# Performance work log

Measured on AMD Instinct MI355X. Metric: run time of the kernel, lower is better.

The kernel has to match this reference:

```python
import jax, jax.numpy as jnp
import numpy as np

DIM = 1024
INTER = 512
E = 32            # n_routed_experts
TOPK = 4          # n_activated_experts
GROUPS = 8        # n_expert_groups
TOPK_GROUPS = 4
SHARED_INTER = 2 * INTER  # n_shared_experts * moe_inter_dim
ROUTE_SCALE = 1.0
B, S = 8, 4096


def setup_inputs() -> dict:
    key = jax.random.key(0)
    ks = jax.random.split(key, 16)
    def xav(k, shape):
        fan_in, fan_out = shape[-2], shape[-1]
        lim = np.sqrt(6.0 / (fan_in + fan_out))
        return jax.random.uniform(k, shape, jnp.float32, -lim, lim)
    return {
        "x": jax.random.normal(ks[0], (B, S, DIM), jnp.float32),
        "gw": xav(ks[1], (DIM, E)),
        "gb": jnp.zeros((E,), jnp.float32),
        "w1": xav(ks[2], (E, DIM, INTER)),
        "b1": jnp.zeros((E, INTER), jnp.float32),
        "w3": xav(ks[3], (E, DIM, INTER)),
        "b3": jnp.zeros((E, INTER), jnp.float32),
        "w2": xav(ks[4], (E, INTER, DIM)),
        "b2": jnp.zeros((E, DIM), jnp.float32),
        "sw1": xav(ks[5], (DIM, SHARED_INTER)),
        "sb1": jnp.zeros((SHARED_INTER,), jnp.float32),
        "sw3": xav(ks[6], (DIM, SHARED_INTER)),
        "sb3": jnp.zeros((SHARED_INTER,), jnp.float32),
        "sw2": xav(ks[7], (SHARED_INTER, DIM)),
        "sb2": jnp.zeros((DIM,), jnp.float32),
    }


def _gate(xf, gw, gb):
    # scores: softmax over routed experts in fp32 (score_func='softmax')
    T = xf.shape[0]
    scores = jax.nn.softmax((xf @ gw + gb).astype(jnp.float32), axis=-1)  # [T, E]
    original_scores = scores
    # group-masked routing (n_expert_groups > 1)
    scores_g = scores.reshape(T, GROUPS, E // GROUPS)                     # [T, G, E/G]
    group_scores = jnp.sum(jax.lax.top_k(scores_g, 2)[0], axis=-1)        # [T, G]
    gidx = jax.lax.top_k(group_scores, TOPK_GROUPS)[1]                    # [T, topk_groups]
    keep = jnp.zeros((T, GROUPS), bool).at[jnp.arange(T)[:, None], gidx].set(True)
    masked = jnp.where(keep[:, :, None], scores_g, -jnp.inf).reshape(T, E)
    indices = jax.lax.top_k(masked, TOPK)[1]                              # [T, topk]
    weights = jnp.take_along_axis(original_scores, indices, axis=1) * ROUTE_SCALE
    return weights.astype(xf.dtype), indices


def reference(x, gw, gb, w1, b1, w3, b3, w2, b2, sw1, sb1, sw3, sb3, sw2, sb2):
    shape = x.shape
    xf = x.reshape(-1, DIM)                                               # [T, dim]
    T = xf.shape[0]
    weights, indices = _gate(xf, gw, gb)
    # dense combine weights [T, E]: w_e(t) = routing weight if expert e chosen for t else 0
    cw = jnp.zeros((T, E), xf.dtype).at[jnp.arange(T)[:, None], indices].add(weights)
    # scan over experts: y += w_e * SwiGLU_e(x). Zero weight -> zero contribution,
    # identical math to the masked dispatch/scatter-add in the torch code.
    def body(y, p):
        w1e, b1e, w3e, b3e, w2e, b2e, we = p
        h = jax.nn.silu(xf @ w1e + b1e) * (xf @ w3e + b3e)                # [T, inter]
        return y + we[:, None] * (h @ w2e + b2e), None
    y0 = jnp.zeros_like(xf)
    y, _ = jax.lax.scan(body, y0, (w1, b1, w3, b3, w2, b2, cw.T))
    # shared experts MLP (SwiGLU)
    z = (jax.nn.silu(xf @ sw1 + sb1) * (xf @ sw3 + sb3)) @ sw2 + sb2
    return (y + z).reshape(shape)
```

## Files before the change

### kernel.cpp

```cpp
#include <hip/hip_runtime.h>
#include <stdint.h>

#define DIM_    1024
#define INTER_  512

typedef short bf16x4 __attribute__((ext_vector_type(4)));
typedef short bf16x8 __attribute__((ext_vector_type(8)));
typedef float f32x4  __attribute__((ext_vector_type(4)));

__device__ __forceinline__ unsigned short f2bf(float f) {
  union { float f; unsigned u; } v; v.f = f;
  return (unsigned short)((v.u + 0x7FFFu + ((v.u >> 16) & 1u)) >> 16);
}
__device__ __forceinline__ unsigned f2bf2(float a, float b) {
  union { float f; unsigned u; } va, vb; va.f = a; vb.f = b;
  unsigned ra = (va.u + 0x7FFFu + ((va.u >> 16) & 1u)) >> 16;
  unsigned rb = (vb.u + 0x7FFFu + ((vb.u >> 16) & 1u)) >> 16;
  return ra | (rb << 16);
}
__device__ __forceinline__ float bfhi(unsigned u) {
  union { unsigned u; float f; } v; v.u = u & 0xffff0000u; return v.f;
}
__device__ __forceinline__ float bflo(unsigned u) {
  union { unsigned u; float f; } v; v.u = u << 16; return v.f;
}

__device__ __forceinline__ void gl16(const void* g, void* l) {
  __builtin_amdgcn_global_load_lds(
      (const __attribute__((address_space(1))) unsigned int*)g,
      (__attribute__((address_space(3))) unsigned int*)l, 16, 0, 0);
}

#define BARX() do { asm volatile("" ::: "memory"); \
                    __builtin_amdgcn_s_barrier();  \
                    asm volatile("" ::: "memory"); } while (0)

__global__ __launch_bounds__(256) void gate_kernel(
    const float* __restrict__ x, const float* __restrict__ gw,
    const float* __restrict__ gb, int* __restrict__ idx, float* __restrict__ wts,
    unsigned short* __restrict__ xb) {
  __shared__ double s_sc[4][32];
  __shared__ double s_gs[4][8];
  const int wid = threadIdx.x >> 6, lane = threadIdx.x & 63;
  const int t = blockIdx.x * 4 + wid;
  {
    const float* xrow = x + (size_t)t * DIM_ + lane * 16;
    unsigned short* xbrow = xb + (size_t)t * DIM_ + lane * 16;
    float4 f0 = *(const float4*)(xrow);
    float4 f1 = *(const float4*)(xrow + 4);
    float4 f2v = *(const float4*)(xrow + 8);
    float4 f3v = *(const float4*)(xrow + 12);
    uint4 o0, o1;
    o0.x = f2bf2(f0.x, f0.y);  o0.y = f2bf2(f0.z, f0.w);
    o0.z = f2bf2(f1.x, f1.y);  o0.w = f2bf2(f1.z, f1.w);
    o1.x = f2bf2(f2v.x, f2v.y); o1.y = f2bf2(f2v.z, f2v.w);
    o1.z = f2bf2(f3v.x, f3v.y); o1.w = f2bf2(f3v.z, f3v.w);
    *(uint4*)(xbrow) = o0;
    *(uint4*)(xbrow + 8) = o1;
  }
  const int e = lane & 31, half = lane >> 5;
  const float* xr  = x  + (size_t)t * DIM_ + half * 512;
  const float* gwp = gw + (size_t)half * 512 * 32 + e;
  double a0 = 0, a1 = 0, a2 = 0, a3 = 0;
  for (int k = 0; k < 512; k += 4) {
    float4 xv = *(const float4*)(xr + k);
    a0 += (double)xv.x * (double)gwp[(k + 0) * 32];
    a1 += (double)xv.y * (double)gwp[(k + 1) * 32];
    a2 += (double)xv.z * (double)gwp[(k + 2) * 32];
    a3 += (double)xv.w * (double)gwp[(k + 3) * 32];
  }
  double lg = (a0 + a1) + (a2 + a3);
  lg += __shfl_xor(lg, 32);
  lg += (double)gb[e];
  double m = lg;
  #pragma unroll
  for (int d = 1; d < 32; d <<= 1) m = fmax(m, __shfl_xor(m, d));
  double ex = exp(lg - m);
  double ssum = ex;
  #pragma unroll
  for (int d = 1; d < 32; d <<= 1) ssum += __shfl_xor(ssum, d);
  double sc = ex / ssum;
  double p  = __shfl_xor(sc, 1);
  double m1 = fmax(sc, p), n1 = fmin(sc, p);
  double m2 = __shfl_xor(m1, 2), n2 = __shfl_xor(n1, 2);
  double gs = (m1 >= m2) ? (m1 + fmax(n1, m2)) : (m2 + fmax(n2, m1));
  if (lane < 32) {
    s_sc[wid][e] = sc;
    if ((e & 3) == 0) s_gs[wid][e >> 2] = gs;
  }
  __syncthreads();
  if (lane == 0) {
    unsigned kmask = 0;
    for (int it = 0; it < 4; ++it) {
      int bg = 0; double bv = -1.0;
      for (int g = 0; g < 8; ++g)
        if (!((kmask >> g) & 1u) && s_gs[wid][g] > bv) { bv = s_gs[wid][g]; bg = g; }
      kmask |= 1u << bg;
    }
    unsigned umask = 0;
    for (int slot = 0; slot < 4; ++slot) {
      int be = 0; double bv = -1.0;
      for (int ee = 0; ee < 32; ++ee)
        if (((kmask >> (ee >> 2)) & 1u) && !((umask >> ee) & 1u) && s_sc[wid][ee] > bv) {
          bv = s_sc[wid][ee]; be = ee;
        }
      umask |= 1u << be;
      idx[t * 4 + slot] = be;
      wts[t * 4 + slot] = (float)bv;
    }
  }
}

__global__ __launch_bounds__(256) void count_kernel(const int* __restrict__ idx,
                                                    int* __restrict__ meta) {
  __shared__ int h[32];
  int tid = threadIdx.x;
  if (tid < 32) h[tid] = 0;
  __syncthreads();
  atomicAdd(&h[idx[blockIdx.x * 256 + tid]], 1);
  __syncthreads();
  if (tid < 32 && h[tid]) atomicAdd(&meta[tid], h[tid]);
}

__global__ void scan_kernel(int* __restrict__ meta) {
  int lane = threadIdx.x & 63;
  if (lane < 32) {
    int c = meta[lane];
    int pre = c;
    #pragma unroll
    for (int d = 1; d < 32; d <<= 1) { int t = __shfl_up(pre, d); if (lane >= d) pre += t; }
    int excl = pre - c;
    meta[64 + lane] = excl;
    meta[32 + lane] = excl;
    int nt = (c + 255) >> 8;
    int ntp = nt;
    #pragma unroll
    for (int d = 1; d < 32; d <<= 1) { int t = __shfl_up(ntp, d); if (lane >= d) ntp += t; }
    int ntExcl = ntp - nt;
    for (int k = 0; k < nt; ++k) { meta[128 + ntExcl + k] = lane; meta[1184 + ntExcl + k] = k << 8; }
    if (lane == 31) { meta[96] = excl + c; meta[97] = ntExcl + nt; }
  }
}

__global__ __launch_bounds__(256) void scatter_kernel(
    const int* __restrict__ idx, int* __restrict__ meta,
    int* __restrict__ tok, int* __restrict__ inv) {
  int i = blockIdx.x * 256 + threadIdx.x;
  int lane = threadIdx.x & 63;
  int e = idx[i];
  unsigned long long m = ~0ull;
  #pragma unroll
  for (int b = 0; b < 5; ++b) {
    unsigned long long vote = __ballot((e >> b) & 1);
    m &= ((e >> b) & 1) ? vote : ~vote;
  }
  int leader = __ffsll((long long)m) - 1;
  int rank = __popcll(m & ((1ull << lane) - 1));
  int base = 0;
  if (lane == leader) base = atomicAdd(&meta[32 + e], (int)__popcll(m));
  base = __shfl(base, leader);
  int p = base + rank;
  tok[p] = i >> 2;
  inv[i] = p;
}

__global__ __launch_bounds__(256) void repack_kernel(
    const float* __restrict__ src, unsigned short* __restrict__ dst,
    int K, int N, int tilesPerMat) {
  const int w = blockIdx.x * 4 + (threadIdx.x >> 6);
  const int j = threadIdx.x & 63;
  const int e = w / tilesPerMat, rem = w % tilesPerMat;
  const int kSteps = K >> 5;
  const int nt = rem / kSteps, kq = rem % kSteps;
  const float* s = src + (size_t)e * K * N + (size_t)(kq * 32) * N + nt * 64 + j;
  float v[32];
  #pragma unroll
  for (int kk = 0; kk < 32; ++kk) v[kk] = s[(size_t)kk * N];
  char* d = (char*)dst + (size_t)w * 4096 + j * 16;
  #pragma unroll
  for (int q = 0; q < 4; ++q) {
    int o = q * 8;
    uint4 tv;
    tv.x = f2bf2(v[o + 0], v[o + 1]);
    tv.y = f2bf2(v[o + 2], v[o + 3]);
    tv.z = f2bf2(v[o + 4], v[o + 5]);
    tv.w = f2bf2(v[o + 6], v[o + 7]);
    *(uint4*)(d + q * 1024) = tv;
  }
}

__global__ __launch_bounds__(256) void repack13_kernel(
    const float* __restrict__ src1, const float* __restrict__ src3,
    unsigned short* __restrict__ dst, int K, int N, int jtTiles) {
  const int w = blockIdx.x * 4 + (threadIdx.x >> 6);
  const int j = threadIdx.x & 63;
  const int kSteps = K >> 5;
  const int tpm = jtTiles * kSteps;
  const int e = w / tpm, rem = w % tpm;
  const int jt = rem / kSteps, kq = rem % kSteps;
  const int jg = jt * 64 + j;
  const int c = ((jg >> 5) << 4) + (jg & 15);
  const float* s = (((jg >> 4) & 1) ? src3 : src1)
                 + (size_t)e * K * N + (size_t)(kq * 32) * N + c;
  float v[32];
  #pragma unroll
  for (int kk = 0; kk < 32; ++kk) v[kk] = s[(size_t)kk * N];
  char* d = (char*)dst + (size_t)w * 4096 + j * 16;
  #pragma unroll
  for (int q = 0; q < 4; ++q) {
    int o = q * 8;
    uint4 tv;
    tv.x = f2bf2(v[o + 0], v[o + 1]);
    tv.y = f2bf2(v[o + 2], v[o + 3]);
    tv.z = f2bf2(v[o + 4], v[o + 5]);
    tv.w = f2bf2(v[o + 6], v[o + 7]);
    *(uint4*)(d + q * 1024) = tv;
  }
}


#define G4_PRE()                                                              \
  const int tid = threadIdx.x, lane = tid & 63, wave = tid >> 6;              \
  const int wm = wave >> 1, wn = wave & 1;                                    \
  const int f = lane & 15, g = lane >> 4;                                     \
  const int rsg = wave * 16 + (lane >> 2);                                    \
  const int qs = (((lane & 3) ^ ((rsg & 3) ^ ((rsg >> 2) & 3))) << 4);        \
  const int wv1k = wave * 1024;                                               \
  const int bso = (wave & 3) * 1024 + lane * 16;                              \
  int aoff[4], boff[4];                                                       \
  _Pragma("unroll")                                                           \
  for (int ii = 0; ii < 4; ++ii) {                                            \
    int u16 = ii * 16 + f;                                                    \
    aoff[ii] = (wm >> 1) * 8192 + (wm & 1) * 4096 + u16 * 64 +                \
               ((g ^ ((u16 & 3) ^ ((u16 >> 2) & 3))) << 4);                   \
    boff[ii] = 16384 + wn * 4096 + g * 1024 + u16 * 16;                       \
  }                                                                           \
  f32x4 acc[4][4];                                                            \
  const f32x4 zz = {0.f, 0.f, 0.f, 0.f};                                      \
  _Pragma("unroll")                                                           \
  for (int mi = 0; mi < 4; ++mi)                                              \
    _Pragma("unroll")                                                         \
    for (int ni = 0; ni < 4; ++ni) acc[mi][ni] = zz;

#define G4_STAGE(td, u_)                                                      \
  gl16(pA0 + (u_) * 64, (td) + wv1k);                                         \
  gl16(pA1 + (u_) * 64, (td) + 8192 + wv1k);                                  \
  gl16(pB + (size_t)(u_) * 4096, (td) + 16384 + wv1k);

#define G4_BODY(NU)                                                           \
  {                                                                           \
    G4_STAGE(lds, 0);                                                         \
    G4_STAGE(lds + 24576, ((NU) > 1 ? 1 : 0));                                \
    asm volatile("s_waitcnt vmcnt(3)" ::: "memory");                          \
    BARX();                                                                   \
  }                                                                           \
  int bc = 0, bt = 49152;                                                     \
  for (int u = 0; u < (NU); ++u) {                                            \
    int u_ = u + 2; if (u_ > (NU) - 1) u_ = (NU) - 1;                         \
    char* td = lds + bt;                                                      \
    G4_STAGE(td, u_);                                                         \
    const char* cb = lds + bc;                                                \
    bf16x8 af[4], bv[4];                                                      \
    _Pragma("unroll")                                                         \
    for (int mi = 0; mi < 4; ++mi) af[mi] = *(const bf16x8*)(cb + aoff[mi]);  \
    _Pragma("unroll")                                                         \
    for (int ni = 0; ni < 4; ++ni) bv[ni] = *(const bf16x8*)(cb + boff[ni]);  \
    __builtin_amdgcn_s_setprio(1);                                            \
    _Pragma("unroll")                                                         \
    for (int ni = 0; ni < 4; ++ni)                                            \
      _Pragma("unroll")                                                       \
      for (int mi = 0; mi < 4; ++mi)                                          \
        acc[mi][ni] = __builtin_amdgcn_mfma_f32_16x16x32_bf16(                \
            af[mi], bv[ni], acc[mi][ni], 0, 0, 0);                            \
    __builtin_amdgcn_s_setprio(0);                                            \
    asm volatile("s_waitcnt vmcnt(3)" ::: "memory");                          \
    BARX();                                                                   \
    bc = (bc == 49152) ? 0 : bc + 24576;                                      \
    bt = (bt == 49152) ? 0 : bt + 24576;                                      \
  }

#define XCD_SWZ(GXv)                                                          \
  const int nb_ = gridDim.x;                                                  \
  const int b_ = blockIdx.x;                                                  \
  const int w_ = (b_ & 7) * (nb_ >> 3) + (b_ >> 3);                           \
  const int bx = w_ % (GXv);                                                  \
  const int by = w_ / (GXv);

__global__ __launch_bounds__(512, 4) void s1_kernel(
    const unsigned short* __restrict__ xb, const unsigned short* __restrict__ w13,
    const float* __restrict__ sb1, const float* __restrict__ sb3,
    unsigned short* __restrict__ Hs) {
  __shared__ char lds[73728];
  XCD_SWZ(16);
  const int m0 = by * 256;
  G4_PRE();
  const char* pA0 = (const char*)xb + (size_t)(m0 + rsg) * 2048 + qs;
  const char* pA1 = pA0 + (size_t)128 * 2048;
  const char* pB = (const char*)w13 + ((size_t)(bx * 2 + (wave >> 2)) * 32) * 4096 + bso;
  G4_BODY(32);
  const int colb = bx * 64;
  #pragma unroll
  for (int p2 = 0; p2 < 2; ++p2) {
    int c = colb + wn * 32 + p2 * 16 + f;
    float bb1 = sb1[c], bb3 = sb3[c];
    #pragma unroll
    for (int mi = 0; mi < 4; ++mi) {
      int row = m0 + wm * 64 + mi * 16 + g * 4;
      #pragma unroll
      for (int r = 0; r < 4; ++r) {
        float v1 = acc[mi][2 * p2][r] + bb1;
        float v3 = acc[mi][2 * p2 + 1][r] + bb3;
        float h = (v1 / (1.f + __expf(-v1))) * v3;
        Hs[(size_t)(row + r) * 1024 + c] = f2bf(h);
      }
    }
  }
}

__global__ __launch_bounds__(512, 4) void s2_kernel(
    const unsigned short* __restrict__ Hs, const unsigned short* __restrict__ b2i,
    const float* __restrict__ sb2, float* __restrict__ out) {
  __shared__ char lds[73728];
  XCD_SWZ(8);
  const int m0 = by * 256;
  G4_PRE();
  const char* pA0 = (const char*)Hs + (size_t)(m0 + rsg) * 2048 + qs;
  const char* pA1 = pA0 + (size_t)128 * 2048;
  const char* pB = (const char*)b2i + ((size_t)(bx * 2 + (wave >> 2)) * 32) * 4096 + bso;
  G4_BODY(32);
  #pragma unroll
  for (int ni = 0; ni < 4; ++ni) {
    int c = bx * 128 + wn * 64 + ni * 16 + f;
    float bb = sb2[c];
    #pragma unroll
    for (int mi = 0; mi < 4; ++mi) {
      int row = m0 + wm * 64 + mi * 16 + g * 4;
      #pragma unroll
      for (int r = 0; r < 4; ++r)
        out[(size_t)(row + r) * 1024 + c] = acc[mi][ni][r] + bb;
    }
  }
}

__global__ __launch_bounds__(512, 4) void g1_kernel(
    const unsigned short* __restrict__ xb, const unsigned short* __restrict__ w13,
    const float* __restrict__ b1, const float* __restrict__ b3,
    const int* __restrict__ tok, const int* __restrict__ meta,
    unsigned short* __restrict__ H) {
  __shared__ char lds[73728];
  XCD_SWZ(8);
  if (by >= meta[97]) return;
  const int e = meta[128 + by], m0 = meta[1184 + by];
  const int off_e = meta[64 + e], nrem = meta[e] - m0;
  G4_PRE();
  const int ix0 = off_e + m0 + ((rsg < nrem) ? rsg : 0);
  const int ix1 = off_e + m0 + ((rsg + 128 < nrem) ? rsg + 128 : 0);
  const char* pA0 = (const char*)xb + (size_t)tok[ix0] * 2048 + qs;
  const char* pA1 = (const char*)xb + (size_t)tok[ix1] * 2048 + qs;
  const char* pB = (const char*)w13 + ((size_t)(e * 16 + bx * 2 + (wave >> 2)) * 32) * 4096 + bso;
  G4_BODY(32);
  const int colb = bx * 64;
  #pragma unroll
  for (int p2 = 0; p2 < 2; ++p2) {
    int c = colb + wn * 32 + p2 * 16 + f;
    float bb1 = b1[e * 512 + c], bb3 = b3[e * 512 + c];
    #pragma unroll
    for (int mi = 0; mi < 4; ++mi) {
      int row = wm * 64 + mi * 16 + g * 4;
      #pragma unroll
      for (int r = 0; r < 4; ++r) {
        if (row + r < nrem) {
          float v1 = acc[mi][2 * p2][r] + bb1;
          float v3 = acc[mi][2 * p2 + 1][r] + bb3;
          float h = (v1 / (1.f + __expf(-v1))) * v3;
          H[(size_t)(off_e + m0 + row + r) * 512 + c] = f2bf(h);
        }
      }
    }
  }
}

__global__ __launch_bounds__(512, 4) void g2_kernel(
    const unsigned short* __restrict__ H, const unsigned short* __restrict__ w2i,
    const float* __restrict__ b2, const int* __restrict__ meta,
    unsigned short* __restrict__ Y, int cbase) {
  __shared__ char lds[73728];
  XCD_SWZ(4);
  if (by >= meta[97]) return;
  const int e = meta[128 + by], m0 = meta[1184 + by];
  const int off_e = meta[64 + e], nrem = meta[e] - m0;
  G4_PRE();
  const int ix0 = off_e + m0 + ((rsg < nrem) ? rsg : 0);
  const int ix1 = off_e + m0 + ((rsg + 128 < nrem) ? rsg + 128 : 0);
  const char* pA0 = (const char*)H + (size_t)ix0 * 1024 + qs;
  const char* pA1 = (const char*)H + (size_t)ix1 * 1024 + qs;
  const int nt0 = (cbase >> 6) + bx * 2;
  const char* pB = (const char*)w2i + ((size_t)(e * 16 + nt0 + (wave >> 2)) * 16) * 4096 + bso;
  G4_BODY(16);
  #pragma unroll
  for (int ni = 0; ni < 4; ++ni) {
    int ycol = bx * 128 + wn * 64 + ni * 16 + f;
    float bb = b2[e * 1024 + cbase + ycol];
    #pragma unroll
    for (int mi = 0; mi < 4; ++mi) {
      int row = wm * 64 + mi * 16 + g * 4;
      #pragma unroll
      for (int r = 0; r < 4; ++r) {
        if (row + r < nrem)
          Y[(size_t)(off_e + m0 + row + r) * 512 + ycol] = f2bf(acc[mi][ni][r] + bb);
      }
    }
  }
}

__global__ __launch_bounds__(256) void combine_kernel(
    const unsigned short* __restrict__ Y, const int* __restrict__ inv,
    const float* __restrict__ wts, float* __restrict__ out, int cbase) {
  int t = blockIdx.x * 2 + (threadIdx.x >> 7);
  int c = (threadIdx.x & 127) * 4;
  int4 iv = *(const int4*)(inv + t * 4);
  float4 wv = *(const float4*)(wts + t * 4);
  float* op = out + (size_t)t * 1024 + cbase + c;
  float4 o = *(float4*)op;
  uint2 u;
  u = *(const uint2*)(Y + (size_t)iv.x * 512 + c);
  o.x += wv.x * bflo(u.x); o.y += wv.x * bfhi(u.x);
  o.z += wv.x * bflo(u.y); o.w += wv.x * bfhi(u.y);
  u = *(const uint2*)(Y + (size_t)iv.y * 512 + c);
  o.x += wv.y * bflo(u.x); o.y += wv.y * bfhi(u.x);
  o.z += wv.y * bflo(u.y); o.w += wv.y * bfhi(u.y);
  u = *(const uint2*)(Y + (size_t)iv.z * 512 + c);
  o.x += wv.z * bflo(u.x); o.y += wv.z * bfhi(u.x);
  o.z += wv.z * bflo(u.y); o.w += wv.z * bfhi(u.y);
  u = *(const uint2*)(Y + (size_t)iv.w * 512 + c);
  o.x += wv.w * bflo(u.x); o.y += wv.w * bfhi(u.x);
  o.z += wv.w * bflo(u.y); o.w += wv.w * bfhi(u.y);
  *(float4*)op = o;
}

extern "C" void kernel_launch(void* const* d_in, const int* in_sizes, int n_in,
                              void* d_out, int out_size, void* d_ws, size_t ws_size,
                              hipStream_t stream) {
  const float* x   = (const float*)d_in[0];
  const float* gw  = (const float*)d_in[1];
  const float* gb  = (const float*)d_in[2];
  const float* w1  = (const float*)d_in[3];
  const float* b1  = (const float*)d_in[4];
  const float* w3  = (const float*)d_in[5];
  const float* b3  = (const float*)d_in[6];
  const float* w2  = (const float*)d_in[7];
  const float* b2  = (const float*)d_in[8];
  const float* sw1 = (const float*)d_in[9];
  const float* sb1 = (const float*)d_in[10];
  const float* sw3 = (const float*)d_in[11];
  const float* sb3 = (const float*)d_in[12];
  const float* sw2 = (const float*)d_in[13];
  const float* sb2 = (const float*)d_in[14];
  float* out = (float*)d_out;
  char* ws = (char*)d_ws;

  const size_t OFF_XB   = 134217728;
  const size_t OFF_W13I = 201326592;
  const size_t OFF_W2I  = 268435456;
  const size_t OFF_S13I = 301989888;
  const size_t OFF_SW2I = 306184192;
  const size_t OFF_IDX  = 308281344;
  const size_t OFF_WTS  = 308805632;
  const size_t OFF_TOK  = 309329920;
  const size_t OFF_INV  = 309854208;
  const size_t OFF_META = 310378496;
  if (ws_size < OFF_META + 8960) return;

  unsigned short* H    = (unsigned short*)ws;
  unsigned short* xb   = (unsigned short*)(ws + OFF_XB);
  unsigned short* Yb   = (unsigned short*)(ws + OFF_XB);
  unsigned short* w13i = (unsigned short*)(ws + OFF_W13I);
  unsigned short* w2i  = (unsigned short*)(ws + OFF_W2I);
  unsigned short* s13i = (unsigned short*)(ws + OFF_S13I);
  unsigned short* sw2i = (unsigned short*)(ws + OFF_SW2I);
  int*   idx  = (int*)(ws + OFF_IDX);
  float* wts  = (float*)(ws + OFF_WTS);
  int*   tokl = (int*)(ws + OFF_TOK);
  int*   inv  = (int*)(ws + OFF_INV);
  int*   meta = (int*)(ws + OFF_META);

  hipMemsetAsync(meta, 0, 128, stream);
  gate_kernel<<<dim3(8192), dim3(256), 0, stream>>>(x, gw, gb, idx, wts, xb);
  count_kernel<<<dim3(512), dim3(256), 0, stream>>>(idx, meta);
  scan_kernel<<<dim3(1), dim3(64), 0, stream>>>(meta);
  scatter_kernel<<<dim3(512), dim3(256), 0, stream>>>(idx, meta, tokl, inv);
  repack13_kernel<<<dim3(4096), dim3(256), 0, stream>>>(w1, w3, w13i, 1024, 512, 16);
  repack_kernel<<<dim3(2048), dim3(256), 0, stream>>>(w2, w2i, 512, 1024, 256);
  repack13_kernel<<<dim3(256), dim3(256), 0, stream>>>(sw1, sw3, s13i, 1024, 1024, 32);
  repack_kernel<<<dim3(128), dim3(256), 0, stream>>>(sw2, sw2i, 1024, 1024, 512);
  s1_kernel<<<dim3(2048), dim3(512), 0, stream>>>(xb, s13i, sb1, sb3, H);
  s2_kernel<<<dim3(1024), dim3(512), 0, stream>>>(H, sw2i, sb2, out);
  g1_kernel<<<dim3(4352), dim3(512), 0, stream>>>(xb, w13i, b1, b3, tokl, meta, H);
  g2_kernel<<<dim3(2176), dim3(512), 0, stream>>>(H, w2i, b2, meta, Yb, 0);
  combine_kernel<<<dim3(16384), dim3(256), 0, stream>>>(Yb, inv, wts, out, 0);
  g2_kernel<<<dim3(2176), dim3(512), 0, stream>>>(H, w2i, b2, meta, Yb, 512);
  combine_kernel<<<dim3(16384), dim3(256), 0, stream>>>(Yb, inv, wts, out, 512);
}
```

Before: 1.399 ms.

## Fuse prep kernels and co-schedule shared and routed expert GEMMs in single launches

Gating and all four weight-repack kernels are merged into one prep launch that dispatches on block index. When the workspace is large enough, the shared-expert up-projection GEMM and the routed-expert up-projection GEMM become one interleaved launch, and so do the shared down-projection and the first half of the routed down-projection. To do this the shared hidden activations move into a separate workspace buffer. The aim is to cut launch gaps and the tail and idle time of each small kernel by letting independent work fill the GPU together, at the cost of more workspace and mixed block types within a launch.

```diff
diff --git a/kernel.cpp b/kernel.cpp
--- a/kernel.cpp
+++ b/kernel.cpp
@@ -35,14 +35,14 @@
                     __builtin_amdgcn_s_barrier();  \
                     asm volatile("" ::: "memory"); } while (0)
 
-__global__ __launch_bounds__(256) void gate_kernel(
-    const float* __restrict__ x, const float* __restrict__ gw,
+__device__ __forceinline__ void gate_body(
+    int bI, const float* __restrict__ x, const float* __restrict__ gw,
     const float* __restrict__ gb, int* __restrict__ idx, float* __restrict__ wts,
     unsigned short* __restrict__ xb) {
   __shared__ double s_sc[4][32];
   __shared__ double s_gs[4][8];
   const int wid = threadIdx.x >> 6, lane = threadIdx.x & 63;
-  const int t = blockIdx.x * 4 + wid;
+  const int t = bI * 4 + wid;
   {
     const float* xrow = x + (size_t)t * DIM_ + lane * 16;
     unsigned short* xbrow = xb + (size_t)t * DIM_ + lane * 16;
@@ -111,63 +111,10 @@
   }
 }
 
-__global__ __launch_bounds__(256) void count_kernel(const int* __restrict__ idx,
-                                                    int* __restrict__ meta) {
-  __shared__ int h[32];
-  int tid = threadIdx.x;
-  if (tid < 32) h[tid] = 0;
-  __syncthreads();
-  atomicAdd(&h[idx[blockIdx.x * 256 + tid]], 1);
-  __syncthreads();
-  if (tid < 32 && h[tid]) atomicAdd(&meta[tid], h[tid]);
-}
-
-__global__ void scan_kernel(int* __restrict__ meta) {
-  int lane = threadIdx.x & 63;
-  if (lane < 32) {
-    int c = meta[lane];
-    int pre = c;
-    #pragma unroll
-    for (int d = 1; d < 32; d <<= 1) { int t = __shfl_up(pre, d); if (lane >= d) pre += t; }
-    int excl = pre - c;
-    meta[64 + lane] = excl;
-    meta[32 + lane] = excl;
-    int nt = (c + 255) >> 8;
-    int ntp = nt;
-    #pragma unroll
-    for (int d = 1; d < 32; d <<= 1) { int t = __shfl_up(ntp, d); if (lane >= d) ntp += t; }
-    int ntExcl = ntp - nt;
-    for (int k = 0; k < nt; ++k) { meta[128 + ntExcl + k] = lane; meta[1184 + ntExcl + k] = k << 8; }
-    if (lane == 31) { meta[96] = excl + c; meta[97] = ntExcl + nt; }
-  }
-}
-
-__global__ __launch_bounds__(256) void scatter_kernel(
-    const int* __restrict__ idx, int* __restrict__ meta,
-    int* __restrict__ tok, int* __restrict__ inv) {
-  int i = blockIdx.x * 256 + threadIdx.x;
-  int lane = threadIdx.x & 63;
-  int e = idx[i];
-  unsigned long long m = ~0ull;
-  #pragma unroll
-  for (int b = 0; b < 5; ++b) {
-    unsigned long long vote = __ballot((e >> b) & 1);
-    m &= ((e >> b) & 1) ? vote : ~vote;
-  }
-  int leader = __ffsll((long long)m) - 1;
-  int rank = __popcll(m & ((1ull << lane) - 1));
-  int base = 0;
-  if (lane == leader) base = atomicAdd(&meta[32 + e], (int)__popcll(m));
-  base = __shfl(base, leader);
-  int p = base + rank;
-  tok[p] = i >> 2;
-  inv[i] = p;
-}
-
-__global__ __launch_bounds__(256) void repack_kernel(
-    const float* __restrict__ src, unsigned short* __restrict__ dst,
+__device__ __forceinline__ void repack_body(
+    int bI, const float* __restrict__ src, unsigned short* __restrict__ dst,
     int K, int N, int tilesPerMat) {
-  const int w = blockIdx.x * 4 + (threadIdx.x >> 6);
+  const int w = bI * 4 + (threadIdx.x >> 6);
   const int j = threadIdx.x & 63;
   const int e = w / tilesPerMat, rem = w % tilesPerMat;
   const int kSteps = K >> 5;
@@ -189,10 +136,10 @@
   }
 }
 
-__global__ __launch_bounds__(256) void repack13_kernel(
-    const float* __restrict__ src1, const float* __restrict__ src3,
+__device__ __forceinline__ void repack13_body(
+    int bI, const float* __restrict__ src1, const float* __restrict__ src3,
     unsigned short* __restrict__ dst, int K, int N, int jtTiles) {
-  const int w = blockIdx.x * 4 + (threadIdx.x >> 6);
+  const int w = bI * 4 + (threadIdx.x >> 6);
   const int j = threadIdx.x & 63;
   const int kSteps = K >> 5;
   const int tpm = jtTiles * kSteps;
@@ -217,7 +164,6 @@
     *(uint4*)(d + q * 1024) = tv;
   }
 }
-
 
 #define G4_PRE()                                                              \
   const int tid = threadIdx.x, lane = tid & 63, wave = tid >> 6;              \
@@ -279,19 +225,15 @@
     bt = (bt == 49152) ? 0 : bt + 24576;                                      \
   }
 
-#define XCD_SWZ(GXv)                                                          \
-  const int nb_ = gridDim.x;                                                  \
-  const int b_ = blockIdx.x;                                                  \
-  const int w_ = (b_ & 7) * (nb_ >> 3) + (b_ >> 3);                           \
-  const int bx = w_ % (GXv);                                                  \
-  const int by = w_ / (GXv);
-
-__global__ __launch_bounds__(512, 4) void s1_kernel(
+__device__ __forceinline__ int2 xcd_swz(int id, int nb, int gx) {
+  int w = (id & 7) * (nb >> 3) + (id >> 3);
+  int2 r; r.x = w % gx; r.y = w / gx; return r;
+}
+
+__device__ __forceinline__ void s1_body(int bx, int by,
     const unsigned short* __restrict__ xb, const unsigned short* __restrict__ w13,
     const float* __restrict__ sb1, const float* __restrict__ sb3,
-    unsigned short* __restrict__ Hs) {
-  __shared__ char lds[73728];
-  XCD_SWZ(16);
+    unsigned short* __restrict__ Hs, char* lds) {
   const int m0 = by * 256;
   G4_PRE();
   const char* pA0 = (const char*)xb + (size_t)(m0 + rsg) * 2048 + qs;
@@ -317,11 +259,9 @@
   }
 }
 
-__global__ __launch_bounds__(512, 4) void s2_kernel(
+__device__ __forceinline__ void s2_body(int bx, int by,
     const unsigned short* __restrict__ Hs, const unsigned short* __restrict__ b2i,
-    const float* __restrict__ sb2, float* __restrict__ out) {
-  __shared__ char lds[73728];
-  XCD_SWZ(8);
+    const float* __restrict__ sb2, float* __restrict__ out, char* lds) {
   const int m0 = by * 256;
   G4_PRE();
   const char* pA0 = (const char*)Hs + (size_t)(m0 + rsg) * 2048 + qs;
@@ -342,13 +282,11 @@
   }
 }
 
-__global__ __launch_bounds__(512, 4) void g1_kernel(
+__device__ __forceinline__ void g1_body(int bx, int by,
     const unsigned short* __restrict__ xb, const unsigned short* __restrict__ w13,
     const float* __restrict__ b1, const float* __restrict__ b3,
     const int* __restrict__ tok, const int* __restrict__ meta,
-    unsigned short* __restrict__ H) {
-  __shared__ char lds[73728];
-  XCD_SWZ(8);
+    unsigned short* __restrict__ H, char* lds) {
   if (by >= meta[97]) return;
   const int e = meta[128 + by], m0 = meta[1184 + by];
   const int off_e = meta[64 + e], nrem = meta[e] - m0;
@@ -380,12 +318,10 @@
   }
 }
 
-__global__ __launch_bounds__(512, 4) void g2_kernel(
+__device__ __forceinline__ void g2_body(int bx, int by,
     const unsigned short* __restrict__ H, const unsigned short* __restrict__ w2i,
     const float* __restrict__ b2, const int* __restrict__ meta,
-    unsigned short* __restrict__ Y, int cbase) {
-  __shared__ char lds[73728];
-  XCD_SWZ(4);
+    unsigned short* __restrict__ Y, int cbase, char* lds) {
   if (by >= meta[97]) return;
   const int e = meta[128 + by], m0 = meta[1184 + by];
   const int off_e = meta[64 + e], nrem = meta[e] - m0;
@@ -410,6 +346,149 @@
           Y[(size_t)(off_e + m0 + row + r) * 512 + ycol] = f2bf(acc[mi][ni][r] + bb);
       }
     }
+  }
+}
+
+__global__ __launch_bounds__(256) void prep_kernel(
+    const float* x, const float* gw, const float* gb, int* idx, float* wts,
+    unsigned short* xb,
+    const float* w1, const float* w3, unsigned short* w13i,
+    const float* w2, unsigned short* w2i,
+    const float* sw1, const float* sw3, unsigned short* s13i,
+    const float* sw2, unsigned short* sw2i) {
+  int b = blockIdx.x;
+  if (b < 8192) { gate_body(b, x, gw, gb, idx, wts, xb); return; }
+  b -= 8192;
+  if (b < 4096) { repack13_body(b, w1, w3, w13i, 1024, 512, 16); return; }
+  b -= 4096;
+  if (b < 2048) { repack_body(b, w2, w2i, 512, 1024, 256); return; }
+  b -= 2048;
+  if (b < 256) { repack13_body(b, sw1, sw3, s13i, 1024, 1024, 32); return; }
+  b -= 256;
+  repack_body(b, sw2, sw2i, 1024, 1024, 512);
+}
+
+__global__ __launch_bounds__(256) void count_kernel(const int* __restrict__ idx,
+                                                    int* __restrict__ meta) {
+  __shared__ int h[32];
+  int tid = threadIdx.x;
+  if (tid < 32) h[tid] = 0;
+  __syncthreads();
+  atomicAdd(&h[idx[blockIdx.x * 256 + tid]], 1);
+  __syncthreads();
+  if (tid < 32 && h[tid]) atomicAdd(&meta[tid], h[tid]);
+}
+
+__global__ void scan_kernel(int* __restrict__ meta) {
+  int lane = threadIdx.x & 63;
+  if (lane < 32) {
+    int c = meta[lane];
+    int pre = c;
+    #pragma unroll
+    for (int d = 1; d < 32; d <<= 1) { int t = __shfl_up(pre, d); if (lane >= d) pre += t; }
+    int excl = pre - c;
+    meta[64 + lane] = excl;
+    meta[32 + lane] = excl;
+    int nt = (c + 255) >> 8;
+    int ntp = nt;
+    #pragma unroll
+    for (int d = 1; d < 32; d <<= 1) { int t = __shfl_up(ntp, d); if (lane >= d) ntp += t; }
+    int ntExcl = ntp - nt;
+    for (int k = 0; k < nt; ++k) { meta[128 + ntExcl + k] = lane; meta[1184 + ntExcl + k] = k << 8; }
+    if (lane == 31) { meta[96] = excl + c; meta[97] = ntExcl + nt; }
+  }
+}
+
+__global__ __launch_bounds__(256) void scatter_kernel(
+    const int* __restrict__ idx, int* __restrict__ meta,
+    int* __restrict__ tok, int* __restrict__ inv) {
+  int i = blockIdx.x * 256 + threadIdx.x;
+  int lane = threadIdx.x & 63;
+  int e = idx[i];
+  unsigned long long m = ~0ull;
+  #pragma unroll
+  for (int b = 0; b < 5; ++b) {
+    unsigned long long vote = __ballot((e >> b) & 1);
+    m &= ((e >> b) & 1) ? vote : ~vote;
+  }
+  int leader = __ffsll((long long)m) - 1;
+  int rank = __popcll(m & ((1ull << lane) - 1));
+  int base = 0;
+  if (lane == leader) base = atomicAdd(&meta[32 + e], (int)__popcll(m));
+  base = __shfl(base, leader);
+  int p = base + rank;
+  tok[p] = i >> 2;
+  inv[i] = p;
+}
+
+__global__ __launch_bounds__(512, 4) void s1_kernel(
+    const unsigned short* xb, const unsigned short* w13,
+    const float* sb1, const float* sb3, unsigned short* Hs) {
+  __shared__ char lds[73728];
+  int2 s = xcd_swz(blockIdx.x, 2048, 16);
+  s1_body(s.x, s.y, xb, w13, sb1, sb3, Hs, lds);
+}
+__global__ __launch_bounds__(512, 4) void s2_kernel(
+    const unsigned short* Hs, const unsigned short* b2i,
+    const float* sb2, float* out) {
+  __shared__ char lds[73728];
+  int2 s = xcd_swz(blockIdx.x, 1024, 8);
+  s2_body(s.x, s.y, Hs, b2i, sb2, out, lds);
+}
+__global__ __launch_bounds__(512, 4) void g1_kernel(
+    const unsigned short* xb, const unsigned short* w13,
+    const float* b1, const float* b3, const int* tok, const int* meta,
+    unsigned short* H) {
+  __shared__ char lds[73728];
+  int2 s = xcd_swz(blockIdx.x, 4352, 8);
+  g1_body(s.x, s.y, xb, w13, b1, b3, tok, meta, H, lds);
+}
+__global__ __launch_bounds__(512, 4) void g2_kernel(
+    const unsigned short* H, const unsigned short* w2i,
+    const float* b2, const int* meta, unsigned short* Y, int cbase) {
+  __shared__ char lds[73728];
+  int2 s = xcd_swz(blockIdx.x, 2176, 4);
+  g2_body(s.x, s.y, H, w2i, b2, meta, Y, cbase, lds);
+}
+
+__global__ __launch_bounds__(512, 4) void s1g1_kernel(
+    const unsigned short* xb, const unsigned short* s13,
+    const float* sb1, const float* sb3, unsigned short* Hs,
+    const unsigned short* w13, const float* b1, const float* b3,
+    const int* tok, const int* meta, unsigned short* H) {
+  __shared__ char lds[73728];
+  int id = blockIdx.x;
+  int type, sub;
+  if (id < 6144) {
+    if (id % 3 == 0) { type = 0; sub = id / 3; }
+    else { type = 1; sub = id - id / 3 - 1; }
+  } else { type = 1; sub = 4096 + (id - 6144); }
+  if (type == 0) {
+    int2 s = xcd_swz(sub, 2048, 16);
+    s1_body(s.x, s.y, xb, s13, sb1, sb3, Hs, lds);
+  } else {
+    int2 s = xcd_swz(sub, 4352, 8);
+    g1_body(s.x, s.y, xb, w13, b1, b3, tok, meta, H, lds);
+  }
+}
+
+__global__ __launch_bounds__(512, 4) void s2g2_kernel(
+    const unsigned short* Hs, const unsigned short* sw2i, const float* sb2,
+    float* out, const unsigned short* H, const unsigned short* w2i,
+    const float* b2, const int* meta, unsigned short* Y) {
+  __shared__ char lds[73728];
+  int id = blockIdx.x;
+  int type, sub;
+  if (id < 3072) {
+    if (id % 3 == 0) { type = 0; sub = id / 3; }
+    else { type = 1; sub = id - id / 3 - 1; }
+  } else { type = 1; sub = 2048 + (id - 3072); }
+  if (type == 0) {
+    int2 s = xcd_swz(sub, 1024, 8);
+    s2_body(s.x, s.y, Hs, sw2i, sb2, out, lds);
+  } else {
+    int2 s = xcd_swz(sub, 2176, 4);
+    g2_body(s.x, s.y, H, w2i, b2, meta, Y, 0, lds);
   }
 }
 
@@ -469,7 +548,11 @@
   const size_t OFF_TOK  = 309329920;
   const size_t OFF_INV  = 309854208;
   const size_t OFF_META = 310378496;
-  if (ws_size < OFF_META + 8960) return;
+  const size_t OFF_HS   = 310394880;
+  const size_t NEED_SMALL = OFF_META + 8960;
+  const size_t NEED_BIG   = OFF_HS + 67108864;
+  if (ws_size < NEED_SMALL) return;
+  const bool big = ws_size >= NEED_BIG;
 
   unsigned short* H    = (unsigned short*)ws;
   unsigned short* xb   = (unsigned short*)(ws + OFF_XB);
@@ -483,21 +566,30 @@
   int*   tokl = (int*)(ws + OFF_TOK);
   int*   inv  = (int*)(ws + OFF_INV);
   int*   meta = (int*)(ws + OFF_META);
+  unsigned short* HsBig = (unsigned short*)(ws + OFF_HS);
 
   hipMemsetAsync(meta, 0, 128, stream);
-  gate_kernel<<<dim3(8192), dim3(256), 0, stream>>>(x, gw, gb, idx, wts, xb);
+  prep_kernel<<<dim3(14720), dim3(256), 0, stream>>>(
+      x, gw, gb, idx, wts, xb, w1, w3, w13i, w2, w2i, sw1, sw3, s13i, sw2, sw2i);
   count_kernel<<<dim3(512), dim3(256), 0, stream>>>(idx, meta);
   scan_kernel<<<dim3(1), dim3(64), 0, stream>>>(meta);
   scatter_kernel<<<dim3(512), dim3(256), 0, stream>>>(idx, meta, tokl, inv);
-  repack13_kernel<<<dim3(4096), dim3(256), 0, stream>>>(w1, w3, w13i, 1024, 512, 16);
-  repack_kernel<<<dim3(2048), dim3(256), 0, stream>>>(w2, w2i, 512, 1024, 256);
-  repack13_kernel<<<dim3(256), dim3(256), 0, stream>>>(sw1, sw3, s13i, 1024, 1024, 32);
-  repack_kernel<<<dim3(128), dim3(256), 0, stream>>>(sw2, sw2i, 1024, 1024, 512);
-  s1_kernel<<<dim3(2048), dim3(512), 0, stream>>>(xb, s13i, sb1, sb3, H);
-  s2_kernel<<<dim3(1024), dim3(512), 0, stream>>>(H, sw2i, sb2, out);
-  g1_kernel<<<dim3(4352), dim3(512), 0, stream>>>(xb, w13i, b1, b3, tokl, meta, H);
-  g2_kernel<<<dim3(2176), dim3(512), 0, stream>>>(H, w2i, b2, meta, Yb, 0);
-  combine_kernel<<<dim3(16384), dim3(256), 0, stream>>>(Yb, inv, wts, out, 0);
-  g2_kernel<<<dim3(2176), dim3(512), 0, stream>>>(H, w2i, b2, meta, Yb, 512);
-  combine_kernel<<<dim3(16384), dim3(256), 0, stream>>>(Yb, inv, wts, out, 512);
-}
+
+  if (big) {
+    s1g1_kernel<<<dim3(6400), dim3(512), 0, stream>>>(
+        xb, s13i, sb1, sb3, HsBig, w13i, b1, b3, tokl, meta, H);
+    s2g2_kernel<<<dim3(3200), dim3(512), 0, stream>>>(
+        HsBig, sw2i, sb2, out, H, w2i, b2, meta, Yb);
+    combine_kernel<<<dim3(16384), dim3(256), 0, stream>>>(Yb, inv, wts, out, 0);
+    g2_kernel<<<dim3(2176), dim3(512), 0, stream>>>(H, w2i, b2, meta, Yb, 512);
+    combine_kernel<<<dim3(16384), dim3(256), 0, stream>>>(Yb, inv, wts, out, 512);
+  } else {
+    s1_kernel<<<dim3(2048), dim3(512), 0, stream>>>(xb, s13i, sb1, sb3, H);
+    s2_kernel<<<dim3(1024), dim3(512), 0, stream>>>(H, sw2i, sb2, out);
+    g1_kernel<<<dim3(4352), dim3(512), 0, stream>>>(xb, w13i, b1, b3, tokl, meta, H);
+    g2_kernel<<<dim3(2176), dim3(512), 0, stream>>>(H, w2i, b2, meta, Yb, 0);
+    combine_kernel<<<dim3(16384), dim3(256), 0, stream>>>(Yb, inv, wts, out, 0);
+    g2_kernel<<<dim3(2176), dim3(512), 0, stream>>>(H, w2i, b2, meta, Yb, 512);
+    combine_kernel<<<dim3(16384), dim3(256), 0, stream>>>(Yb, inv, wts, out, 512);
+  }
+}
```

New measurement: 1.320 ms, median of 2. 1.06x faster.
